# Optimization experiments

Hardware: AMD Instinct MI355X
Metric: run time of the kernel (lower is better)

Reference implementation:

```python
import jax, jax.numpy as jnp
import numpy as np

B, S, HID = 1, 2048, 4096
H, KV, D, R = 32, 8, 128, 64   # heads, kv heads, head_dim, rotary_dim
EPS = 1e-6
THETA = 10000.0


def setup_inputs() -> dict:
    key = jax.random.key(0)
    ks = jax.random.split(key, 6)
    sc = 0.02
    return {
        'hidden_states': jax.random.normal(ks[0], (B, S, HID), jnp.float32),
        'Wq': jax.random.normal(ks[1], (H * D, HID), jnp.float32) * sc,
        'Wk': jax.random.normal(ks[2], (KV * D, HID), jnp.float32) * sc,
        'Wv': jax.random.normal(ks[3], (KV * D, HID), jnp.float32) * sc,
        'Wo': jax.random.normal(ks[4], (HID, H * D), jnp.float32) * sc,
        'q_norm_w': jnp.ones((H * D,), jnp.float32),
        'k_norm_w': jnp.ones((KV * D,), jnp.float32),
        'position_ids': jnp.broadcast_to(jnp.arange(S, dtype=jnp.int64)[None, :], (B, S)),
    }


def _rms_norm(x, w):
    xf = x.astype(jnp.float32)
    var = jnp.mean(xf * xf, axis=-1, keepdims=True)
    return (w * (xf * jax.lax.rsqrt(var + EPS))).astype(x.dtype)


def _rotate_half(x):
    x1, x2 = x[..., : R // 2], x[..., R // 2:]
    return jnp.concatenate((-x2, x1), axis=-1)


def reference(hidden_states, Wq, Wk, Wv, Wo, q_norm_w, k_norm_w, position_ids):
    x = hidden_states
    # projections (torch Linear: y = x @ W^T)
    q = jnp.einsum('bsd,od->bso', x, Wq)                      # [B,S,H*D]
    k = jnp.einsum('bsd,od->bso', x, Wk)                      # [B,S,KV*D]
    v = jnp.einsum('bsd,od->bso', x, Wv).reshape(B, S, KV, D)
    # QK RMSNorm over flattened head dims
    q = _rms_norm(q, q_norm_w).reshape(B, S, H, D)
    k = _rms_norm(k, k_norm_w).reshape(B, S, KV, D)
    # partial RoPE: rotary_dim=R out of head_dim=D
    inv_freq = 1.0 / (THETA ** (jnp.arange(0, R, 2, dtype=jnp.float32) / R))  # [R/2]
    freqs = position_ids.astype(jnp.float32)[..., None] * inv_freq            # [B,S,R/2]
    emb = jnp.concatenate((freqs, freqs), axis=-1)                            # [B,S,R]
    cos = jnp.cos(emb)[:, :, None, :]                                         # [B,S,1,R]
    sin = jnp.sin(emb)[:, :, None, :]
    q_rot = q[..., :R] * cos + _rotate_half(q[..., :R]) * sin
    k_rot = k[..., :R] * cos + _rotate_half(k[..., :R]) * sin
    q = jnp.concatenate((q_rot, q[..., R:]), axis=-1)
    k = jnp.concatenate((k_rot, k[..., R:]), axis=-1)
    # GQA repeat_kv
    G = H // KV
    k = jnp.repeat(k, G, axis=2)  # [B,S,H,D]
    v = jnp.repeat(v, G, axis=2)
    # attention with causal mask, softmax in fp32
    scaling = D ** -0.5
    scores = jnp.einsum('bqhd,bkhd->bhqk', q, k) * scaling    # [B,H,S,S]
    causal = jnp.tril(jnp.ones((S, S), dtype=bool))
    scores = jnp.where(causal[None, None], scores, jnp.finfo(jnp.float32).min)
    attn = jax.nn.softmax(scores.astype(jnp.float32), axis=-1).astype(q.dtype)
    out = jnp.einsum('bhqk,bkhd->bqhd', attn, v).reshape(B, S, H * D)
    return jnp.einsum('bso,do->bsd', out, Wo)
```

## Files before the change

kernel.cpp:

```cpp
#include <hip/hip_runtime.h>
#include <hip/hip_bf16.h>
#include <math.h>

typedef __bf16 bf16;
typedef __bf16 bf16x8 __attribute__((ext_vector_type(8)));
typedef float f32x4 __attribute__((ext_vector_type(4)));

#define S_LEN 2048
#define HID_D 4096
#define NH 32
#define NKV 8
#define HD 128
#define SCALE_LOG2 (0.08838834764831843f * 1.4426950408889634f)
#define FIXED_M 17.0f

__device__ __forceinline__ void gload_lds16(const void* g, void* lds) {
  __builtin_amdgcn_global_load_lds((__attribute__((address_space(1))) void*)g,
                                   (__attribute__((address_space(3))) void*)lds, 16, 0, 0);
}

#define MEMFENCE asm volatile("" ::: "memory")

__global__ __launch_bounds__(256) void cvt_kernel(const float* __restrict__ in,
                                                  bf16* __restrict__ out, int n8) {
  int i = blockIdx.x * blockDim.x + threadIdx.x;
  int stride = gridDim.x * blockDim.x;
  for (; i < n8; i += stride) {
    const float4* p = (const float4*)in + 2 * (size_t)i;
    float4 a = p[0], b = p[1];
    bf16x8 o;
    o[0] = (bf16)a.x; o[1] = (bf16)a.y; o[2] = (bf16)a.z; o[3] = (bf16)a.w;
    o[4] = (bf16)b.x; o[5] = (bf16)b.y; o[6] = (bf16)b.z; o[7] = (bf16)b.w;
    *((bf16x8*)out + i) = o;
  }
}

template <int BM, int BN>
__global__ __launch_bounds__(512, 2) void gemm_s(const bf16* __restrict__ A,
                                                 const bf16* __restrict__ B,
                                                 float* __restrict__ C,
                                                 int N, int Kfull, int T) {
  constexpr int MFr = BM / 32;
  constexpr int NFr = BN / 64;
  constexpr int NL = (BM + BN) / 64;
  constexpr int TILE = (BM + BN) * 128;

  __shared__ __align__(16) char lds[2 * TILE];
  const int t = threadIdx.x, l = t & 63, w = t >> 6;
  const int wr = w >> 2, wc = w & 3;
  const int l15 = l & 15, lg = l >> 4;

  const int GX = gridDim.x, GY = gridDim.y;
  const int lin = blockIdx.y * GX + blockIdx.x;
  const int x = lin & 7, j = lin >> 3;
  const int rectW = GX >> 2, rectH = GY >> 1;
  const int rx = x & 3, ry = x >> 2;
  const int jn = j % rectW, jm = j / rectW;
  const int n0 = (rx * rectW + jn) * BN;
  const int m0 = (ry * rectH + jm) * BM;

  auto stage = [&](int d, int tau) {
    char* dst = lds + d * TILE;
    const size_t kpos = (size_t)tau * 64;
#pragma unroll
    for (int i = 0; i < NL; i++) {
      int q = i * 512 + t;
      int r = q >> 3;
      int c = (q & 7) ^ (r & 7);
      const bf16* src = (i * 512 < BM * 8)
                            ? (A + (size_t)(m0 + r) * Kfull)
                            : (B + (size_t)(n0 + (r - BM)) * Kfull);
      gload_lds16(src + kpos + c * 8, dst + q * 16);
    }
  };

  f32x4 acc[MFr][NFr] = {};

  stage(0, 0);
  asm volatile("s_waitcnt vmcnt(0)" ::: "memory");
  MEMFENCE; __builtin_amdgcn_s_barrier(); MEMFENCE;

  for (int tau = 0; tau < T; tau++) {
    const int d = tau & 1;
    if (tau + 1 < T) stage(d ^ 1, tau + 1);

    const char* Ab = lds + d * TILE;
    const char* Bb = Ab + BM * 128;
    bf16x8 a[MFr][2], b[NFr][2];
#pragma unroll
    for (int mf = 0; mf < MFr; mf++) {
      const int row = wr * (BM / 2) + mf * 16 + l15;
#pragma unroll
      for (int ks = 0; ks < 2; ks++)
        a[mf][ks] = *(const bf16x8*)(Ab + row * 128 + (((ks * 4 + lg) ^ (row & 7)) << 4));
    }
#pragma unroll
    for (int nf = 0; nf < NFr; nf++) {
      const int row = wc * (BN / 4) + nf * 16 + l15;
#pragma unroll
      for (int ks = 0; ks < 2; ks++)
        b[nf][ks] = *(const bf16x8*)(Bb + row * 128 + (((ks * 4 + lg) ^ (row & 7)) << 4));
    }
#pragma unroll
    for (int mf = 0; mf < MFr; mf++)
#pragma unroll
      for (int nf = 0; nf < NFr; nf++)
#pragma unroll
        for (int ks = 0; ks < 2; ks++)
          acc[mf][nf] = __builtin_amdgcn_mfma_f32_16x16x32_bf16(a[mf][ks], b[nf][ks],
                                                               acc[mf][nf], 0, 0, 0);

    asm volatile("s_waitcnt vmcnt(0)" ::: "memory");
    MEMFENCE; __builtin_amdgcn_s_barrier(); MEMFENCE;
  }

#pragma unroll
  for (int mf = 0; mf < MFr; mf++) {
    int row = m0 + wr * (BM / 2) + mf * 16 + lg * 4;
#pragma unroll
    for (int nf = 0; nf < NFr; nf++) {
      int col = n0 + wc * (BN / 4) + nf * 16 + l15;
      float* Cp = C + (size_t)row * N + col;
#pragma unroll
      for (int rr = 0; rr < 4; rr++) Cp[(size_t)rr * N] = acc[mf][nf][rr];
    }
  }
}

__global__ __launch_bounds__(256) void vt_kernel(const float* __restrict__ QKV,
                                                 bf16* __restrict__ Vt) {
  __shared__ __align__(16) float tile[64][68];
  const int s0 = blockIdx.x * 64, d0 = blockIdx.y * 64;
  const int t = threadIdx.x;
#pragma unroll
  for (int i = 0; i < 4; i++) {
    int row = i * 16 + (t >> 4);
    int c4 = t & 15;
    float4 v = *(const float4*)(QKV + (size_t)(s0 + row) * 6144 + 5120 + d0 + c4 * 4);
    *(float4*)&tile[row][c4 * 4] = v;
  }
  __syncthreads();
#pragma unroll
  for (int i = 0; i < 2; i++) {
    int slot = i * 256 + t;
    int dr = slot >> 3, ch = slot & 7;
    bf16x8 o;
#pragma unroll
    for (int j = 0; j < 8; j++) o[j] = (bf16)tile[ch * 8 + j][dr];
    *(bf16x8*)(Vt + (size_t)(d0 + dr) * S_LEN + s0 + ch * 8) = o;
  }
}

__global__ __launch_bounds__(256) void prep_kernel(const float* __restrict__ QKV,
                                                   const float* __restrict__ qw,
                                                   const float* __restrict__ kw,
                                                   const int* __restrict__ pos_ids,
                                                   bf16* __restrict__ Qb,
                                                   bf16* __restrict__ Kb) {
  __shared__ __align__(16) float row[5120];
  __shared__ float cs[64];
  __shared__ float red[8];
  const int s = blockIdx.x, t = threadIdx.x;

  const float4* src = (const float4*)(QKV + (size_t)s * 6144);
#pragma unroll
  for (int i = 0; i < 5; i++) ((float4*)row)[t + i * 256] = src[t + i * 256];

  if (t < 32) {
    float p = (float)pos_ids[s];
    float ang = p * powf(10000.0f, -(float)t * (1.0f / 32.0f));
    float sn, cn;
    sincosf(ang, &sn, &cn);
    cs[t] = cn;
    cs[32 + t] = sn;
  }
  __syncthreads();

  float aq = 0.f, ak = 0.f;
  for (int i = t; i < 4096; i += 256) { float v = row[i]; aq += v * v; }
  for (int i = 4096 + t; i < 5120; i += 256) { float v = row[i]; ak += v * v; }
#pragma unroll
  for (int off = 32; off; off >>= 1) {
    aq += __shfl_down(aq, off);
    ak += __shfl_down(ak, off);
  }
  if ((t & 63) == 0) { red[t >> 6] = aq; red[4 + (t >> 6)] = ak; }
  __syncthreads();
  const float scq = rsqrtf((red[0] + red[1] + red[2] + red[3]) * (1.0f / 4096.0f) + 1e-6f);
  const float sck = rsqrtf((red[4] + red[5] + red[6] + red[7]) * (1.0f / 1024.0f) + 1e-6f);

  for (int e = t; e < 4096; e += 256) {
    int d = e & 127;
    int hh = e >> 7;
    float val = row[e] * scq * qw[e];
    float o;
    if (d < 32)       o = val * cs[d] - (row[e + 32] * scq * qw[e + 32]) * cs[32 + d];
    else if (d < 64)  o = val * cs[d - 32] + (row[e - 32] * scq * qw[e - 32]) * cs[d];
    else              o = val;
    Qb[((size_t)hh * S_LEN + s) * HD + d] = (bf16)o;
  }
  for (int e = t; e < 1024; e += 256) {
    int d = e & 127;
    int hh = e >> 7;
    int ri = 4096 + e;
    float val = row[ri] * sck * kw[e];
    float o;
    if (d < 32)       o = val * cs[d] - (row[ri + 32] * sck * kw[e + 32]) * cs[32 + d];
    else if (d < 64)  o = val * cs[d - 32] + (row[ri - 32] * sck * kw[e - 32]) * cs[d];
    else              o = val;
    Kb[((size_t)hh * S_LEN + s) * HD + d] = (bf16)o;
  }
}

__global__ __launch_bounds__(256, 2) void attn_kernel(const bf16* __restrict__ Qb,
                                                      const bf16* __restrict__ Kb,
                                                      const bf16* __restrict__ Vt,
                                                      bf16* __restrict__ Ctx) {
  __shared__ __align__(16) char KB[2][16384];
  __shared__ __align__(16) char VB[2][16384];
  __shared__ __align__(16) char PB[8192];
  const int t = threadIdx.x, l = t & 63, w = t >> 6;
  const int l15 = l & 15, lg = l >> 4;
  const int pairc = blockIdx.x >> 5;
  const int h = blockIdx.x & 31;

  const bf16* Kh = Kb + (size_t)(h >> 2) * S_LEN * HD;
  const bf16* Vh = Vt + (size_t)(h >> 2) * HD * S_LEN;
  char* Pw = PB + w * 2048;

  const int kj0 = t & 15;
  const int vj0 = t & 7;

  auto stageK = [&](int buf, int kvbase) {
#pragma unroll
    for (int i = 0; i < 4; i++) {
      int r = (i * 256 + t) >> 4;
      const bf16* src = Kh + (size_t)(kvbase + r) * HD + ((kj0 ^ (r & 7)) << 3);
      gload_lds16(src, KB[buf] + (i * 256 + w * 64) * 16);
    }
  };
  auto stageV = [&](int buf, int kvbase) {
#pragma unroll
    for (int i = 0; i < 4; i++) {
      int r = (i * 256 + t) >> 3;
      const bf16* src = Vh + (size_t)r * S_LEN + kvbase + ((vj0 ^ (r & 7)) << 3);
      gload_lds16(src, VB[buf] + (i * 256 + w * 64) * 16);
    }
  };

#pragma unroll
  for (int phase = 0; phase < 2; phase++) {
    const int chunk = (phase == 0) ? pairc : (31 - pairc);
    const int ktiles = chunk + 1;
    const int q0 = chunk * 64 + w * 16;

    const bf16* Qh = Qb + ((size_t)h * S_LEN + q0) * HD;
    bf16x8 qf[4];
#pragma unroll
    for (int kk = 0; kk < 4; kk++)
      qf[kk] = *(const bf16x8*)(Qh + (size_t)l15 * HD + kk * 32 + lg * 8);

    stageK(0, 0);
    stageV(0, 0);

    f32x4 O[8] = {};
    float lsum[4] = {0.f, 0.f, 0.f, 0.f};

    for (int tt = 0; tt < ktiles; tt++) {
      const int cur = tt & 1;
      const int kv0 = tt * 64;
      const char* Kcur = KB[cur];
      const bool hasnext = (tt + 1 < ktiles);

      asm volatile("s_waitcnt vmcnt(0)" ::: "memory");
      MEMFENCE;
      __builtin_amdgcn_s_barrier();
      MEMFENCE;

      f32x4 sc[4];
#pragma unroll
      for (int g = 0; g < 4; g++) sc[g] = (f32x4){0.f, 0.f, 0.f, 0.f};
      __builtin_amdgcn_s_setprio(1);
#pragma unroll
      for (int g = 0; g < 4; g++) {
        const int r = g * 16 + l15;
        const char* Krow = Kcur + r * 256;
        const int sw = (r & 7);
#pragma unroll
        for (int kk = 0; kk < 4; kk++) {
          bf16x8 kf = *(const bf16x8*)(Krow + (((kk * 4 + lg) ^ sw) << 4));
          sc[g] = __builtin_amdgcn_mfma_f32_16x16x32_bf16(qf[kk], kf, sc[g], 0, 0, 0);
        }
      }
      __builtin_amdgcn_s_setprio(0);

      if (hasnext) {
        stageK(cur ^ 1, kv0 + 64);
        stageV(cur ^ 1, kv0 + 64);
      }

      const bool needmask = (kv0 + 63 > q0);
      float sv[4][4];
#pragma unroll
      for (int g = 0; g < 4; g++)
#pragma unroll
        for (int r = 0; r < 4; r++) {
          float x = fmaf(sc[g][r], SCALE_LOG2, -FIXED_M);
          if (needmask) {
            int kv = kv0 + g * 16 + l15;
            int qr = q0 + lg * 4 + r;
            if (kv > qr) x = -1e30f;
          }
          sv[g][r] = exp2f(x);
        }
#pragma unroll
      for (int r = 0; r < 4; r++)
        lsum[r] += (sv[0][r] + sv[1][r]) + (sv[2][r] + sv[3][r]);

#pragma unroll
      for (int g = 0; g < 4; g++)
#pragma unroll
        for (int r = 0; r < 4; r++) {
          int prow = lg * 4 + r;
          int csw = (prow & 3) ^ (((prow >> 2) & 3) << 1);
          int pbyte = prow * 128 + (((g * 16 + l15) * 2) ^ (csw << 4));
          *(bf16*)(Pw + pbyte) = (bf16)sv[g][r];
        }
      asm volatile("s_waitcnt lgkmcnt(0)" ::: "memory");
      const int rcsw = (l15 & 3) ^ (((l15 >> 2) & 3) << 1);
      bf16x8 pa[2];
#pragma unroll
      for (int ks = 0; ks < 2; ks++)
        pa[ks] = *(const bf16x8*)(Pw + l15 * 128 + (((ks * 4 + lg) ^ rcsw) << 4));

      __builtin_amdgcn_s_setprio(1);
#pragma unroll
      for (int ks = 0; ks < 2; ks++)
#pragma unroll
        for (int dt = 0; dt < 8; dt++) {
          const int r = dt * 16 + l15;
          bf16x8 vf = *(const bf16x8*)(VB[cur] + r * 128 + (((ks * 4 + lg) ^ (r & 7)) << 4));
          O[dt] = __builtin_amdgcn_mfma_f32_16x16x32_bf16(pa[ks], vf, O[dt], 0, 0, 0);
        }
      __builtin_amdgcn_s_setprio(0);
    }

    MEMFENCE;
    __builtin_amdgcn_s_barrier();
    MEMFENCE;

#pragma unroll
    for (int r = 0; r < 4; r++) {
      float x = lsum[r];
      x += __shfl_xor(x, 1);
      x += __shfl_xor(x, 2);
      x += __shfl_xor(x, 4);
      x += __shfl_xor(x, 8);
      float inv = 1.0f / x;
      bf16* Cp = Ctx + (size_t)(q0 + lg * 4 + r) * HID_D + h * HD + l15;
#pragma unroll
      for (int dt = 0; dt < 8; dt++) Cp[dt * 16] = (bf16)(O[dt][r] * inv);
    }
  }
}

extern "C" void kernel_launch(void* const* d_in, const int* in_sizes, int n_in,
                              void* d_out, int out_size, void* d_ws, size_t ws_size,
                              hipStream_t stream) {
  const float* X  = (const float*)d_in[0];
  const float* Wq = (const float*)d_in[1];
  const float* Wk = (const float*)d_in[2];
  const float* Wv = (const float*)d_in[3];
  const float* Wo = (const float*)d_in[4];
  const float* qw = (const float*)d_in[5];
  const float* kw = (const float*)d_in[6];
  const int* pos  = (const int*)d_in[7];

  char* ws = (char*)d_ws;
  bf16* Xb    = (bf16*)ws;
  bf16* Wqkvb = (bf16*)(ws + (16ll << 20));
  bf16* Wob   = Wqkvb;
  float* QKV  = (float*)(ws + (64ll << 20));
  bf16* Ctx   = (bf16*)(ws + (96ll << 20));
  bf16* Qb    = (bf16*)(ws + (112ll << 20));
  bf16* Kb    = (bf16*)(ws + (128ll << 20));
  bf16* Vt    = (bf16*)(ws + (132ll << 20));

  cvt_kernel<<<2048, 256, 0, stream>>>(X, Xb, S_LEN * HID_D / 8);
  cvt_kernel<<<2048, 256, 0, stream>>>(Wq, Wqkvb, 4096 * 4096 / 8);
  cvt_kernel<<<512, 256, 0, stream>>>(Wk, Wqkvb + 4096 * 4096, 1024 * 4096 / 8);
  cvt_kernel<<<512, 256, 0, stream>>>(Wv, Wqkvb + 5120 * 4096, 1024 * 4096 / 8);

  gemm_s<128, 384><<<dim3(16, 16), 512, 0, stream>>>(Xb, Wqkvb, QKV, 6144, HID_D, 64);

  cvt_kernel<<<2048, 256, 0, stream>>>(Wo, Wob, 4096 * 4096 / 8);

  vt_kernel<<<dim3(32, 16), 256, 0, stream>>>(QKV, Vt);
  prep_kernel<<<S_LEN, 256, 0, stream>>>(QKV, qw, kw, pos, Qb, Kb);

  attn_kernel<<<dim3(512), 256, 0, stream>>>(Qb, Kb, Vt, Ctx);

  gemm_s<128, 256><<<dim3(16, 16), 512, 0, stream>>>(Ctx, Wob, (float*)d_out,
                                                     HID_D, HID_D, 64);
}
```

Baseline: 315.8 us.

## Switch attention to 32x32x16 MFMA with 128-row query blocks

Rewrites the attention kernel to use 32x32x16 bf16 MFMA instead of 16x16x32. Each wave now owns 32 query rows and each block 128, with the grid halved to 256 blocks. V is single-buffered and staged after the barrier, with finer vmcnt waits and an extra barrier per tile. The larger MFMA tile cuts LDS fragment reads per FLOP, but the half-size grid (256 blocks on a 256-CU part), the extra barriers and the higher register pressure from the 16-element accumulators may reduce occupancy and overlap.

```diff
diff --git a/kernel.cpp b/kernel.cpp
--- a/kernel.cpp
+++ b/kernel.cpp
@@ -5,6 +5,7 @@
 typedef __bf16 bf16;
 typedef __bf16 bf16x8 __attribute__((ext_vector_type(8)));
 typedef float f32x4 __attribute__((ext_vector_type(4)));
+typedef float f32x16 __attribute__((ext_vector_type(16)));
 
 #define S_LEN 2048
 #define HID_D 4096
@@ -217,16 +218,16 @@
                                                       const bf16* __restrict__ Vt,
                                                       bf16* __restrict__ Ctx) {
   __shared__ __align__(16) char KB[2][16384];
-  __shared__ __align__(16) char VB[2][16384];
-  __shared__ __align__(16) char PB[8192];
+  __shared__ __align__(16) char VB[16384];
+  __shared__ __align__(16) char PB[16384];
   const int t = threadIdx.x, l = t & 63, w = t >> 6;
-  const int l15 = l & 15, lg = l >> 4;
+  const int l31 = l & 31, hi = l >> 5;
   const int pairc = blockIdx.x >> 5;
   const int h = blockIdx.x & 31;
 
   const bf16* Kh = Kb + (size_t)(h >> 2) * S_LEN * HD;
   const bf16* Vh = Vt + (size_t)(h >> 2) * HD * S_LEN;
-  char* Pw = PB + w * 2048;
+  char* Pw = PB + w * 4096;
 
   const int kj0 = t & 15;
   const int vj0 = t & 7;
@@ -239,32 +240,31 @@
       gload_lds16(src, KB[buf] + (i * 256 + w * 64) * 16);
     }
   };
-  auto stageV = [&](int buf, int kvbase) {
+  auto stageV = [&](int kvbase) {
 #pragma unroll
     for (int i = 0; i < 4; i++) {
       int r = (i * 256 + t) >> 3;
       const bf16* src = Vh + (size_t)r * S_LEN + kvbase + ((vj0 ^ (r & 7)) << 3);
-      gload_lds16(src, VB[buf] + (i * 256 + w * 64) * 16);
+      gload_lds16(src, VB + (i * 256 + w * 64) * 16);
     }
   };
 
 #pragma unroll
   for (int phase = 0; phase < 2; phase++) {
-    const int chunk = (phase == 0) ? pairc : (31 - pairc);
-    const int ktiles = chunk + 1;
-    const int q0 = chunk * 64 + w * 16;
+    const int chunk = (phase == 0) ? pairc : (15 - pairc);
+    const int ktiles = 2 * chunk + 2;
+    const int q0 = chunk * 128 + w * 32;
 
     const bf16* Qh = Qb + ((size_t)h * S_LEN + q0) * HD;
-    bf16x8 qf[4];
-#pragma unroll
-    for (int kk = 0; kk < 4; kk++)
-      qf[kk] = *(const bf16x8*)(Qh + (size_t)l15 * HD + kk * 32 + lg * 8);
+    bf16x8 qf[8];
+#pragma unroll
+    for (int j = 0; j < 8; j++)
+      qf[j] = *(const bf16x8*)(Qh + (size_t)l31 * HD + j * 16 + hi * 8);
 
     stageK(0, 0);
-    stageV(0, 0);
-
-    f32x4 O[8] = {};
-    float lsum[4] = {0.f, 0.f, 0.f, 0.f};
+
+    f32x16 O[4] = {};
+    float lsum[16] = {};
 
     for (int tt = 0; tt < ktiles; tt++) {
       const int cur = tt & 1;
@@ -272,76 +272,77 @@
       const char* Kcur = KB[cur];
       const bool hasnext = (tt + 1 < ktiles);
 
-      asm volatile("s_waitcnt vmcnt(0)" ::: "memory");
       MEMFENCE;
       __builtin_amdgcn_s_barrier();
       MEMFENCE;
 
-      f32x4 sc[4];
-#pragma unroll
-      for (int g = 0; g < 4; g++) sc[g] = (f32x4){0.f, 0.f, 0.f, 0.f};
+      stageV(kv0);
+      if (hasnext) {
+        stageK(cur ^ 1, kv0 + 64);
+        asm volatile("s_waitcnt vmcnt(8)" ::: "memory");
+      } else {
+        asm volatile("s_waitcnt vmcnt(4)" ::: "memory");
+      }
+      MEMFENCE;
+      __builtin_amdgcn_s_barrier();
+      MEMFENCE;
+
+      f32x16 sc[2] = {};
       __builtin_amdgcn_s_setprio(1);
 #pragma unroll
-      for (int g = 0; g < 4; g++) {
-        const int r = g * 16 + l15;
-        const char* Krow = Kcur + r * 256;
-        const int sw = (r & 7);
-#pragma unroll
-        for (int kk = 0; kk < 4; kk++) {
-          bf16x8 kf = *(const bf16x8*)(Krow + (((kk * 4 + lg) ^ sw) << 4));
-          sc[g] = __builtin_amdgcn_mfma_f32_16x16x32_bf16(qf[kk], kf, sc[g], 0, 0, 0);
+      for (int n = 0; n < 2; n++) {
+        const int kr = n * 32 + l31;
+        const char* Krow = Kcur + kr * 256;
+        const int sw = l31 & 7;
+#pragma unroll
+        for (int j = 0; j < 8; j++) {
+          bf16x8 kf = *(const bf16x8*)(Krow + (((2 * j + hi) ^ sw) << 4));
+          sc[n] = __builtin_amdgcn_mfma_f32_32x32x16_bf16(qf[j], kf, sc[n], 0, 0, 0);
         }
       }
       __builtin_amdgcn_s_setprio(0);
 
-      if (hasnext) {
-        stageK(cur ^ 1, kv0 + 64);
-        stageV(cur ^ 1, kv0 + 64);
+      const bool needmask = (kv0 + 63 > q0);
+#pragma unroll
+      for (int n = 0; n < 2; n++) {
+        const int kv = kv0 + n * 32 + l31;
+#pragma unroll
+        for (int e = 0; e < 16; e++) {
+          const int row = (e & 3) + 8 * (e >> 2) + 4 * hi;
+          float x = fmaf(sc[n][e], SCALE_LOG2, -FIXED_M);
+          if (needmask && kv > q0 + row) x = -1e30f;
+          float sv = exp2f(x);
+          lsum[e] += sv;
+          const int chunkc = 4 * n + (l31 >> 3);
+          *(bf16*)(Pw + row * 128 + (((chunkc ^ (row & 7))) << 4) + ((l31 & 7) << 1)) =
+              (bf16)sv;
+        }
       }
-
-      const bool needmask = (kv0 + 63 > q0);
-      float sv[4][4];
-#pragma unroll
-      for (int g = 0; g < 4; g++)
-#pragma unroll
-        for (int r = 0; r < 4; r++) {
-          float x = fmaf(sc[g][r], SCALE_LOG2, -FIXED_M);
-          if (needmask) {
-            int kv = kv0 + g * 16 + l15;
-            int qr = q0 + lg * 4 + r;
-            if (kv > qr) x = -1e30f;
-          }
-          sv[g][r] = exp2f(x);
+      asm volatile("s_waitcnt lgkmcnt(0)" ::: "memory");
+
+      bf16x8 pa[4];
+#pragma unroll
+      for (int j = 0; j < 4; j++)
+        pa[j] = *(const bf16x8*)(Pw + l31 * 128 + (((2 * j + hi) ^ (l31 & 7)) << 4));
+
+      if (hasnext) asm volatile("s_waitcnt vmcnt(4)" ::: "memory");
+      else         asm volatile("s_waitcnt vmcnt(0)" ::: "memory");
+      MEMFENCE;
+      __builtin_amdgcn_s_barrier();
+      MEMFENCE;
+
+      __builtin_amdgcn_s_setprio(1);
+#pragma unroll
+      for (int dt = 0; dt < 4; dt++) {
+        const int vr = dt * 32 + l31;
+        const char* Vrow = VB + vr * 128;
+        const int sw = l31 & 7;
+#pragma unroll
+        for (int j = 0; j < 4; j++) {
+          bf16x8 vf = *(const bf16x8*)(Vrow + (((2 * j + hi) ^ sw) << 4));
+          O[dt] = __builtin_amdgcn_mfma_f32_32x32x16_bf16(pa[j], vf, O[dt], 0, 0, 0);
         }
-#pragma unroll
-      for (int r = 0; r < 4; r++)
-        lsum[r] += (sv[0][r] + sv[1][r]) + (sv[2][r] + sv[3][r]);
-
-#pragma unroll
-      for (int g = 0; g < 4; g++)
-#pragma unroll
-        for (int r = 0; r < 4; r++) {
-          int prow = lg * 4 + r;
-          int csw = (prow & 3) ^ (((prow >> 2) & 3) << 1);
-          int pbyte = prow * 128 + (((g * 16 + l15) * 2) ^ (csw << 4));
-          *(bf16*)(Pw + pbyte) = (bf16)sv[g][r];
-        }
-      asm volatile("s_waitcnt lgkmcnt(0)" ::: "memory");
-      const int rcsw = (l15 & 3) ^ (((l15 >> 2) & 3) << 1);
-      bf16x8 pa[2];
-#pragma unroll
-      for (int ks = 0; ks < 2; ks++)
-        pa[ks] = *(const bf16x8*)(Pw + l15 * 128 + (((ks * 4 + lg) ^ rcsw) << 4));
-
-      __builtin_amdgcn_s_setprio(1);
-#pragma unroll
-      for (int ks = 0; ks < 2; ks++)
-#pragma unroll
-        for (int dt = 0; dt < 8; dt++) {
-          const int r = dt * 16 + l15;
-          bf16x8 vf = *(const bf16x8*)(VB[cur] + r * 128 + (((ks * 4 + lg) ^ (r & 7)) << 4));
-          O[dt] = __builtin_amdgcn_mfma_f32_16x16x32_bf16(pa[ks], vf, O[dt], 0, 0, 0);
-        }
+      }
       __builtin_amdgcn_s_setprio(0);
     }
 
@@ -349,18 +350,24 @@
     __builtin_amdgcn_s_barrier();
     MEMFENCE;
 
-#pragma unroll
-    for (int r = 0; r < 4; r++) {
-      float x = lsum[r];
+    float inv[16];
+#pragma unroll
+    for (int e = 0; e < 16; e++) {
+      float x = lsum[e];
       x += __shfl_xor(x, 1);
       x += __shfl_xor(x, 2);
       x += __shfl_xor(x, 4);
       x += __shfl_xor(x, 8);
-      float inv = 1.0f / x;
-      bf16* Cp = Ctx + (size_t)(q0 + lg * 4 + r) * HID_D + h * HD + l15;
-#pragma unroll
-      for (int dt = 0; dt < 8; dt++) Cp[dt * 16] = (bf16)(O[dt][r] * inv);
-    }
+      x += __shfl_xor(x, 16);
+      inv[e] = 1.0f / x;
+    }
+#pragma unroll
+    for (int dt = 0; dt < 4; dt++)
+#pragma unroll
+      for (int e = 0; e < 16; e++) {
+        const int row = (e & 3) + 8 * (e >> 2) + 4 * hi;
+        Ctx[(size_t)(q0 + row) * HID_D + h * HD + dt * 32 + l31] = (bf16)(O[dt][e] * inv[e]);
+      }
   }
 }
 
@@ -398,7 +405,7 @@
   vt_kernel<<<dim3(32, 16), 256, 0, stream>>>(QKV, Vt);
   prep_kernel<<<S_LEN, 256, 0, stream>>>(QKV, qw, kw, pos, Qb, Kb);
 
-  attn_kernel<<<dim3(512), 256, 0, stream>>>(Qb, Kb, Vt, Ctx);
+  attn_kernel<<<dim3(256), 256, 0, stream>>>(Qb, Kb, Vt, Ctx);
 
   gemm_s<128, 256><<<dim3(16, 16), 512, 0, stream>>>(Ctx, Wob, (float*)d_out,
                                                      HID_D, HID_D, 64);
```

New measurement: 359.7 us. 13.9% more time.
